# Optimization experiments

Hardware: AMD Instinct MI355X
Metric: run time of the kernel (lower is better)

## Reference

```python
import jax, jax.numpy as jnp
import numpy as np

N_EMBED = 1024
HEAD_SIZE = 64
BLOCK_SIZE = 2048

def setup_inputs() -> dict:
    key = jax.random.key(0)
    kx, kq, kk, kv = jax.random.split(key, 4)
    scale = N_EMBED ** -0.5
    x = jax.random.normal(kx, (8, 2048, N_EMBED), dtype=jnp.float32)
    # nn.Linear weights stored as [out, in]; we keep [in, out] for x @ W
    Wq = jax.random.normal(kq, (N_EMBED, HEAD_SIZE), dtype=jnp.float32) * scale
    Wk = jax.random.normal(kk, (N_EMBED, HEAD_SIZE), dtype=jnp.float32) * scale
    Wv = jax.random.normal(kv, (N_EMBED, HEAD_SIZE), dtype=jnp.float32) * scale
    return {"x": x, "Wq": Wq, "Wk": Wk, "Wv": Wv}

def reference(x, Wq, Wk, Wv):
    B, T, C = x.shape
    q = x @ Wq  # [B,T,H]
    k = x @ Wk
    v = x @ Wv
    # NOTE: original scales by C**-0.5 (n_embed), not head_size**-0.5
    wei = jnp.einsum('bth,bsh->bts', q, k) * (C ** -0.5)  # [B,T,T]
    causal = jnp.tril(jnp.ones((T, T), dtype=bool))
    wei = jnp.where(causal, wei, -jnp.inf)
    wei = jax.nn.softmax(wei, axis=-1)
    out = jnp.einsum('bts,bsh->bth', wei, v)  # [B,T,H]
    return out
```

## Files before the change

### kernel.cpp

```cpp
#include <hip/hip_runtime.h>

#define B_ 8
#define T_ 2048
#define C_ 1024
#define H_ 64

typedef __attribute__((ext_vector_type(8))) short short8;
typedef __attribute__((ext_vector_type(4))) float floatx4;
typedef __attribute__((ext_vector_type(4))) int intx4;

static __device__ __forceinline__ unsigned short f2bf(float f) {
  unsigned int u = __builtin_bit_cast(unsigned int, f);
  u += 0x7FFFu + ((u >> 16) & 1u);
  return (unsigned short)(u >> 16);
}
static __device__ __forceinline__ unsigned short f2bf_t(float f) {
  return (unsigned short)(__builtin_bit_cast(unsigned int, f) >> 16);
}
static __device__ __forceinline__ float bf2f(unsigned short u) {
  return __builtin_bit_cast(float, ((unsigned int)u) << 16);
}
static __device__ __forceinline__ unsigned int fbits(float f) {
  return __builtin_bit_cast(unsigned int, f);
}

typedef const __attribute__((address_space(1))) unsigned int* gp1_t;
typedef __attribute__((address_space(3))) unsigned int* lp3_t;
static __device__ __forceinline__ void gl_lds16(const void* g, void* l) {
  __builtin_amdgcn_global_load_lds((gp1_t)g, (lp3_t)l, 16, 0, 0);
}

__global__ __launch_bounds__(256) void conv_w(const float* __restrict__ wq,
    const float* __restrict__ wk, const float* __restrict__ wv,
    unsigned short* __restrict__ wf) {
  int c = blockIdx.x * 256 + threadIdx.x;
  int lane = c & 63;
  int t = c >> 6;
  int ng = t % 12;
  int kk = t / 12;
  int k0 = kk * 32 + (lane >> 4) * 8;
  int n = ng * 16 + (lane & 15);
  const float* src;
  int col;
  float scale = 1.0f;
  if (n < 64)       { src = wq; col = n;       scale = 0.03125f * 1.44269504088896340736f; }
  else if (n < 128) { src = wk; col = n - 64;  }
  else              { src = wv; col = n - 128; }
  unsigned short o[8];
#pragma unroll
  for (int j = 0; j < 8; ++j) o[j] = f2bf(src[(size_t)(k0 + j) * H_ + col] * scale);
  *(uint4*)&wf[(size_t)c * 8] = *(const uint4*)o;
}

__global__ __launch_bounds__(256, 4) void qkv_proj(
    const float* __restrict__ x, const unsigned short* __restrict__ wf,
    unsigned short* __restrict__ qo, unsigned short* __restrict__ kf,
    unsigned short* __restrict__ vf) {
  __shared__ float XL[2][4096];
  int tid = threadIdx.x;
  int wave = tid >> 6, lane = tid & 63;
  int lane4 = lane & 15, quad = lane >> 4;
  int m0 = blockIdx.x * 32;
  int ph0 = blockIdx.x & 7;

  auto stage_ph = [&](int phr, int buf) {
#pragma unroll
    for (int j = 0; j < 4; ++j) {
      int c = (wave * 4 + j) * 64 + lane;
      int r = c >> 5, pc = c & 31;
      int cl = (pc & ~7) | ((pc ^ (r & 7)) & 7);
      gl_lds16(&x[(size_t)(m0 + r) * C_ + phr * 128 + cl * 4], &XL[buf][c * 4]);
    }
  };

  floatx4 acc[2][3];
#pragma unroll
  for (int mt = 0; mt < 2; ++mt)
#pragma unroll
    for (int nt = 0; nt < 3; ++nt) acc[mt][nt] = (floatx4)0.0f;

  stage_ph(ph0, 0);
  __syncthreads();

  for (int ph = 0; ph < 8; ++ph) {
    int buf = ph & 1;
    if (ph < 7) stage_ph((ph + 1 + ph0) & 7, buf ^ 1);
    int phr = (ph + ph0) & 7;
#pragma unroll
    for (int sl = 0; sl < 4; ++sl) {
      int s = phr * 4 + sl;
      short8 b[3];
#pragma unroll
      for (int nt = 0; nt < 3; ++nt)
        b[nt] = *(const short8*)&wf[(size_t)(s * 12 + wave * 3 + nt) * 512 + lane * 8];
      short8 a[2];
#pragma unroll
      for (int mt = 0; mt < 2; ++mt) {
        int r = mt * 16 + lane4;
        int c0 = sl * 8 + quad * 2;
        int pc0 = (c0 & ~7) | ((c0 ^ (r & 7)) & 7);
        int pc1 = ((c0 + 1) & ~7) | (((c0 + 1) ^ (r & 7)) & 7);
        float4 f0 = *(const float4*)&XL[buf][r * 128 + pc0 * 4];
        float4 f1 = *(const float4*)&XL[buf][r * 128 + pc1 * 4];
        intx4 pk;
        pk[0] = (int)__builtin_amdgcn_perm(fbits(f0.y), fbits(f0.x), 0x07060302u);
        pk[1] = (int)__builtin_amdgcn_perm(fbits(f0.w), fbits(f0.z), 0x07060302u);
        pk[2] = (int)__builtin_amdgcn_perm(fbits(f1.y), fbits(f1.x), 0x07060302u);
        pk[3] = (int)__builtin_amdgcn_perm(fbits(f1.w), fbits(f1.z), 0x07060302u);
        a[mt] = __builtin_bit_cast(short8, pk);
      }
#pragma unroll
      for (int mt = 0; mt < 2; ++mt)
#pragma unroll
        for (int nt = 0; nt < 3; ++nt)
          acc[mt][nt] = __builtin_amdgcn_mfma_f32_16x16x32_bf16(a[mt], b[nt], acc[mt][nt], 0, 0, 0);
    }
    __syncthreads();
  }

  unsigned short* VTB = (unsigned short*)&XL[0][0];
  unsigned short* KB  = VTB + 5120;
#pragma unroll
  for (int mt = 0; mt < 2; ++mt)
#pragma unroll
    for (int nt = 0; nt < 3; ++nt) {
      int n = wave * 48 + nt * 16 + lane4;
#pragma unroll
      for (int rr = 0; rr < 4; ++rr) {
        unsigned short val = f2bf(acc[mt][nt][rr]);
        int lrow = mt * 16 + quad * 4 + rr;
        if (n < 64)       qo[(size_t)(m0 + lrow) * H_ + n] = val;
        else if (n < 128) KB[lrow * 72 + (n - 64)] = val;
        else              VTB[(n - 128) * 40 + lrow] = val;
      }
    }
  __syncthreads();
  {
    int bb = m0 >> 11, t0 = m0 & 2047;
    int st = t0 >> 6, off = t0 & 63;
    int ks = tid >> 7, ctl = (tid >> 6) & 1, ln = tid & 63;
    int ct = (off >> 4) + ctl;
    int tl = ctl * 16 + (ln & 15);
    int h0 = ks * 32 + (ln >> 4) * 8;
    uint4 kd = *(const uint4*)&KB[tl * 72 + h0];
    *(uint4*)&kf[((size_t)((bb * 32 + st) * 2 + ks) * 4 + ct) * 512 + ln * 8] = kd;
    int nt = tid >> 6, l4 = tid & 15, qs = (tid >> 4) & 3;
    int ksv = off >> 5;
    uint4 vd = *(const uint4*)&VTB[(nt * 16 + l4) * 40 + qs * 8];
    *(uint4*)&vf[((size_t)((bb * 32 + st) * 2 + ksv) * 4 + nt) * 512 + (tid & 63) * 8] = vd;
  }
}

__global__ __launch_bounds__(256) void attn(
    const unsigned short* __restrict__ qi, const unsigned short* __restrict__ Kf,
    const unsigned short* __restrict__ Vf, unsigned short* __restrict__ Op,
    float* __restrict__ lsum) {
  __shared__ unsigned short KV[2][8192];
  __shared__ unsigned short PL[4][16][72];

  int tid = threadIdx.x;
  int wave = tid >> 6, lane = tid & 63;
  int lane4 = lane & 15, quad = lane >> 4;
  int qt = 31 - (int)blockIdx.x;
  int b = blockIdx.y, split = blockIdx.z;
  int qb = qt * 64;
  int base = b * T_;

  int ntile = qt + 1;
  int sBeg = (split * ntile) >> 2;
  int sEnd = ((split + 1) * ntile) >> 2;

  short8 aq[2];
#pragma unroll
  for (int ks = 0; ks < 2; ++ks)
    aq[ks] = *(const short8*)&qi[(size_t)(base + qb + wave * 16 + lane4) * H_ + ks * 32 + quad * 8];

  float lrow[4];
  floatx4 o[4];
#pragma unroll
  for (int r = 0; r < 4; ++r) lrow[r] = 0.0f;
#pragma unroll
  for (int nt = 0; nt < 4; ++nt) o[nt] = (floatx4)0.0f;

  auto stage = [&](int st, int bf) {
    const unsigned short* ksrc = &Kf[(size_t)(b * 32 + st) * 4096];
    const unsigned short* vsrc = &Vf[(size_t)(b * 32 + st) * 4096];
#pragma unroll
    for (int j = 0; j < 4; ++j) {
      int c = j * 256 + tid;
      const unsigned short* src = (j < 2) ? &ksrc[c * 8] : &vsrc[c * 8 - 4096];
      gl_lds16(src, &KV[bf][c * 8]);
    }
  };

  if (sBeg < sEnd) stage(sBeg, 0);
  __syncthreads();

  for (int st = sBeg; st < sEnd; ++st) {
    int buf = (st - sBeg) & 1;
    if (st + 1 < sEnd) stage(st + 1, buf ^ 1);

    short8 bk[2][4];
#pragma unroll
    for (int ks = 0; ks < 2; ++ks)
#pragma unroll
      for (int ct = 0; ct < 4; ++ct)
        bk[ks][ct] = *(const short8*)&KV[buf][(ks * 4 + ct) * 512 + lane * 8];

    floatx4 sacc[4];
#pragma unroll
    for (int ct = 0; ct < 4; ++ct) sacc[ct] = (floatx4)0.0f;
#pragma unroll
    for (int ks = 0; ks < 2; ++ks)
#pragma unroll
      for (int ct = 0; ct < 4; ++ct)
        sacc[ct] = __builtin_amdgcn_mfma_f32_16x16x32_bf16(aq[ks], bk[ks][ct], sacc[ct], 0, 0, 0);

    if (st == qt) {
#pragma unroll
      for (int ct = 0; ct < 4; ++ct)
#pragma unroll
        for (int r = 0; r < 4; ++r) {
          int qrow = wave * 16 + quad * 4 + r;
          int scol = ct * 16 + lane4;
          if (scol > qrow) sacc[ct][r] = -3.0e38f;
        }
    }

#pragma unroll
    for (int ct = 0; ct < 4; ++ct)
#pragma unroll
      for (int r = 0; r < 4; ++r) {
        float p = exp2f(sacc[ct][r] - 8.0f);
        lrow[r] += p;
        PL[wave][quad * 4 + r][ct * 16 + lane4] = f2bf_t(p);
      }

#pragma unroll
    for (int ks = 0; ks < 2; ++ks) {
      short8 pa = *(const short8*)&PL[wave][lane4][ks * 32 + quad * 8];
      short8 bv[4];
#pragma unroll
      for (int nt = 0; nt < 4; ++nt)
        bv[nt] = *(const short8*)&KV[buf][4096 + (ks * 4 + nt) * 512 + lane * 8];
#pragma unroll
      for (int nt = 0; nt < 4; ++nt)
        o[nt] = __builtin_amdgcn_mfma_f32_16x16x32_bf16(pa, bv[nt], o[nt], 0, 0, 0);
    }

    __syncthreads();
  }

#pragma unroll
  for (int off = 1; off < 16; off <<= 1)
#pragma unroll
    for (int r = 0; r < 4; ++r) lrow[r] += __shfl_xor(lrow[r], off);

  size_t pbase = (((size_t)split * 8 + b) * 32 + qt) * 64;
#pragma unroll
  for (int r = 0; r < 4; ++r) {
    int row = wave * 16 + quad * 4 + r;
#pragma unroll
    for (int nt = 0; nt < 4; ++nt)
      Op[(pbase + row) * 64 + nt * 16 + lane4] = f2bf(o[nt][r]);
    if (lane4 == 0) lsum[pbase + row] = lrow[r];
  }
}

__global__ __launch_bounds__(256) void merge_splits(
    const unsigned short* __restrict__ Op, const float* __restrict__ lsum,
    float* __restrict__ out) {
  int idx = blockIdx.x * 256 + threadIdx.x;
  int row = idx >> 4;
  int h4 = (idx & 15) * 4;
  int b = row >> 11, t = row & 2047;
  int qt = t >> 6, r = t & 63;
  float O0 = 0.f, O1 = 0.f, O2 = 0.f, O3 = 0.f, l = 0.f;
#pragma unroll
  for (int s = 0; s < 4; ++s) {
    size_t p = (((size_t)s * 8 + b) * 32 + qt) * 64 + r;
    l += lsum[p];
    ushort4 ov = *(const ushort4*)&Op[p * 64 + h4];
    O0 += bf2f(ov.x); O1 += bf2f(ov.y); O2 += bf2f(ov.z); O3 += bf2f(ov.w);
  }
  float inv = 1.0f / l;
  float4 res = make_float4(O0 * inv, O1 * inv, O2 * inv, O3 * inv);
  *(float4*)&out[(size_t)row * H_ + h4] = res;
}

extern "C" void kernel_launch(void* const* d_in, const int* in_sizes, int n_in,
                              void* d_out, int out_size, void* d_ws, size_t ws_size,
                              hipStream_t stream) {
  const float* x  = (const float*)d_in[0];
  const float* wq = (const float*)d_in[1];
  const float* wk = (const float*)d_in[2];
  const float* wv = (const float*)d_in[3];
  float* out = (float*)d_out;

  char* ws = (char*)d_ws;
  unsigned short* wf = (unsigned short*)ws;
  unsigned short* qb = (unsigned short*)(ws + 393216);
  unsigned short* kf = (unsigned short*)(ws + 2490368);
  unsigned short* vf = (unsigned short*)(ws + 4587520);
  unsigned short* Op = (unsigned short*)(ws + 6684672);
  float*          ls = (float*)(ws + 15073280);

  conv_w<<<96, 256, 0, stream>>>(wq, wk, wv, wf);
  qkv_proj<<<512, 256, 0, stream>>>(x, wf, qb, kf, vf);
  attn<<<dim3(32, 8, 4), 256, 0, stream>>>(qb, kf, vf, Op, ls);
  merge_splits<<<1024, 256, 0, stream>>>(Op, ls, out);
}
```

Baseline: 130.6 us.

## Use 128-row query tiles with 8 waves sharing each staged K/V tile

The attention kernel now launches 512-thread blocks covering 128 query rows each, so every K/V tile staged into LDS is reused by twice as many waves and global-to-LDS traffic per query row is halved. The causal mask is generalised to the last two key tiles, and the split and merge indexing is changed to match the 128-row layout. K/V fragment loads are interleaved with the MFMAs, and the MFMA sections are wrapped in s_setprio raises. The trade-off is half as many blocks, a coarser causal-imbalance granularity, and more LDS per block.

```diff
diff --git a/kernel.cpp b/kernel.cpp
--- a/kernel.cpp
+++ b/kernel.cpp
@@ -151,22 +151,22 @@
   }
 }
 
-__global__ __launch_bounds__(256) void attn(
+__global__ __launch_bounds__(512, 4) void attn(
     const unsigned short* __restrict__ qi, const unsigned short* __restrict__ Kf,
     const unsigned short* __restrict__ Vf, unsigned short* __restrict__ Op,
     float* __restrict__ lsum) {
   __shared__ unsigned short KV[2][8192];
-  __shared__ unsigned short PL[4][16][72];
+  __shared__ unsigned short PL[8][16][72];
 
   int tid = threadIdx.x;
   int wave = tid >> 6, lane = tid & 63;
   int lane4 = lane & 15, quad = lane >> 4;
-  int qt = 31 - (int)blockIdx.x;
+  int qt = 15 - (int)blockIdx.x;
   int b = blockIdx.y, split = blockIdx.z;
-  int qb = qt * 64;
+  int qb = qt * 128;
   int base = b * T_;
 
-  int ntile = qt + 1;
+  int ntile = 2 * qt + 2;
   int sBeg = (split * ntile) >> 2;
   int sEnd = ((split + 1) * ntile) >> 2;
 
@@ -183,14 +183,9 @@
   for (int nt = 0; nt < 4; ++nt) o[nt] = (floatx4)0.0f;
 
   auto stage = [&](int st, int bf) {
-    const unsigned short* ksrc = &Kf[(size_t)(b * 32 + st) * 4096];
-    const unsigned short* vsrc = &Vf[(size_t)(b * 32 + st) * 4096];
-#pragma unroll
-    for (int j = 0; j < 4; ++j) {
-      int c = j * 256 + tid;
-      const unsigned short* src = (j < 2) ? &ksrc[c * 8] : &vsrc[c * 8 - 4096];
-      gl_lds16(src, &KV[bf][c * 8]);
-    }
+    size_t tb = (size_t)(b * 32 + st) * 4096;
+    gl_lds16(&Kf[tb + (size_t)tid * 8], &KV[bf][tid * 8]);
+    gl_lds16(&Vf[tb + (size_t)tid * 8], &KV[bf][4096 + tid * 8]);
   };
 
   if (sBeg < sEnd) stage(sBeg, 0);
@@ -200,29 +195,26 @@
     int buf = (st - sBeg) & 1;
     if (st + 1 < sEnd) stage(st + 1, buf ^ 1);
 
-    short8 bk[2][4];
+    floatx4 sacc[4];
+#pragma unroll
+    for (int ct = 0; ct < 4; ++ct) sacc[ct] = (floatx4)0.0f;
+    __builtin_amdgcn_s_setprio(1);
 #pragma unroll
     for (int ks = 0; ks < 2; ++ks)
 #pragma unroll
+      for (int ct = 0; ct < 4; ++ct) {
+        short8 bk = *(const short8*)&KV[buf][(ks * 4 + ct) * 512 + lane * 8];
+        sacc[ct] = __builtin_amdgcn_mfma_f32_16x16x32_bf16(aq[ks], bk, sacc[ct], 0, 0, 0);
+      }
+    __builtin_amdgcn_s_setprio(0);
+
+    if (st >= 2 * qt) {
+#pragma unroll
       for (int ct = 0; ct < 4; ++ct)
-        bk[ks][ct] = *(const short8*)&KV[buf][(ks * 4 + ct) * 512 + lane * 8];
-
-    floatx4 sacc[4];
-#pragma unroll
-    for (int ct = 0; ct < 4; ++ct) sacc[ct] = (floatx4)0.0f;
-#pragma unroll
-    for (int ks = 0; ks < 2; ++ks)
-#pragma unroll
-      for (int ct = 0; ct < 4; ++ct)
-        sacc[ct] = __builtin_amdgcn_mfma_f32_16x16x32_bf16(aq[ks], bk[ks][ct], sacc[ct], 0, 0, 0);
-
-    if (st == qt) {
-#pragma unroll
-      for (int ct = 0; ct < 4; ++ct)
 #pragma unroll
         for (int r = 0; r < 4; ++r) {
-          int qrow = wave * 16 + quad * 4 + r;
-          int scol = ct * 16 + lane4;
+          int qrow = qb + wave * 16 + quad * 4 + r;
+          int scol = st * 64 + ct * 16 + lane4;
           if (scol > qrow) sacc[ct][r] = -3.0e38f;
         }
     }
@@ -236,17 +228,17 @@
         PL[wave][quad * 4 + r][ct * 16 + lane4] = f2bf_t(p);
       }
 
+    __builtin_amdgcn_s_setprio(1);
 #pragma unroll
     for (int ks = 0; ks < 2; ++ks) {
       short8 pa = *(const short8*)&PL[wave][lane4][ks * 32 + quad * 8];
-      short8 bv[4];
-#pragma unroll
-      for (int nt = 0; nt < 4; ++nt)
-        bv[nt] = *(const short8*)&KV[buf][4096 + (ks * 4 + nt) * 512 + lane * 8];
-#pragma unroll
-      for (int nt = 0; nt < 4; ++nt)
-        o[nt] = __builtin_amdgcn_mfma_f32_16x16x32_bf16(pa, bv[nt], o[nt], 0, 0, 0);
-    }
+#pragma unroll
+      for (int nt = 0; nt < 4; ++nt) {
+        short8 bv = *(const short8*)&KV[buf][4096 + (ks * 4 + nt) * 512 + lane * 8];
+        o[nt] = __builtin_amdgcn_mfma_f32_16x16x32_bf16(pa, bv, o[nt], 0, 0, 0);
+      }
+    }
+    __builtin_amdgcn_s_setprio(0);
 
     __syncthreads();
   }
@@ -256,7 +248,7 @@
 #pragma unroll
     for (int r = 0; r < 4; ++r) lrow[r] += __shfl_xor(lrow[r], off);
 
-  size_t pbase = (((size_t)split * 8 + b) * 32 + qt) * 64;
+  size_t pbase = (((size_t)split * 8 + b) * 16 + qt) * 128;
 #pragma unroll
   for (int r = 0; r < 4; ++r) {
     int row = wave * 16 + quad * 4 + r;
@@ -274,11 +266,11 @@
   int row = idx >> 4;
   int h4 = (idx & 15) * 4;
   int b = row >> 11, t = row & 2047;
-  int qt = t >> 6, r = t & 63;
+  int qt = t >> 7, r = t & 127;
   float O0 = 0.f, O1 = 0.f, O2 = 0.f, O3 = 0.f, l = 0.f;
 #pragma unroll
   for (int s = 0; s < 4; ++s) {
-    size_t p = (((size_t)s * 8 + b) * 32 + qt) * 64 + r;
+    size_t p = (((size_t)s * 8 + b) * 16 + qt) * 128 + r;
     l += lsum[p];
     ushort4 ov = *(const ushort4*)&Op[p * 64 + h4];
     O0 += bf2f(ov.x); O1 += bf2f(ov.y); O2 += bf2f(ov.z); O3 += bf2f(ov.w);
@@ -307,6 +299,6 @@
 
   conv_w<<<96, 256, 0, stream>>>(wq, wk, wv, wf);
   qkv_proj<<<512, 256, 0, stream>>>(x, wf, qb, kf, vf);
-  attn<<<dim3(32, 8, 4), 256, 0, stream>>>(qb, kf, vf, Op, ls);
+  attn<<<dim3(16, 8, 4), 512, 0, stream>>>(qb, kf, vf, Op, ls);
   merge_splits<<<1024, 256, 0, stream>>>(Op, ls, out);
 }
```

Result: faster. 128.0 us (-2.0%).
